# Kernel tuning notes

Measured on AMD Instinct MI355X. Metric: run time of the kernel, lower is better.

The kernel has to match this reference:

```python
import jax, jax.numpy as jnp
import numpy as np

BS, SL, INDIM, D, H = 2, 2048, 1024, 64, 16
DH = D * H


def _rotation_buffers(sl, units):
    # int rotation_values branch: values=arange(sl), min_lam=1, max_lam=1000
    half = units // 2
    min_lam, max_lam = 1.0, 1000.0
    theta = min_lam / (2.0 * np.pi) * (max_lam / min_lam) ** (2.0 * np.arange(half) / units)
    pos = np.arange(sl, dtype=np.float64)[:, None] / theta[None]  # [sl, half]
    # tile([...,2]).reshape == repeat each entry twice along last dim -> [sl, units]
    rcos = np.repeat(np.cos(pos), 2, axis=-1).astype(np.float32)
    rsin = np.repeat(np.sin(pos), 2, axis=-1).astype(np.float32)
    return jnp.asarray(rcos), jnp.asarray(rsin)


def setup_inputs() -> dict:
    key = jax.random.key(0)
    ks = jax.random.split(key, 8)
    s = 0.02
    x = jax.random.normal(ks[0], (BS, SL, INDIM), jnp.float32)
    mask = jnp.zeros((BS, SL), jnp.float32)  # subtracted from logits; zeros = no masking
    Wqkv = jax.random.normal(ks[1], (INDIM, 3 * DH), jnp.float32) * s
    bqkv = jnp.zeros((3 * DH,), jnp.float32)
    Wo = jax.random.normal(ks[2], (DH, INDIM), jnp.float32) * s
    bo = jnp.zeros((INDIM,), jnp.float32)
    Wg = jax.random.normal(ks[3], (INDIM, DH), jnp.float32) * s
    bg = jnp.zeros((DH,), jnp.float32)
    Wb = jax.random.normal(ks[4], (INDIM, H), jnp.float32) * s
    bb = jnp.zeros((H,), jnp.float32)
    alphaq = jnp.zeros((), jnp.float32)
    alphak = jnp.zeros((), jnp.float32)
    alphav = jnp.zeros((), jnp.float32)
    rcos, rsin = _rotation_buffers(SL, D)
    return dict(x=x, mask=mask, Wqkv=Wqkv, bqkv=bqkv, Wo=Wo, bo=bo, Wg=Wg, bg=bg,
                Wb=Wb, bb=bb, alphaq=alphaq, alphak=alphak, alphav=alphav,
                rcos=rcos, rsin=rsin)


def _rotate(X, cos, sin_even):
    # Faithful to the in-place torch code:
    #   X_ = X*cos; X_[...,::2] += -sin[...,::2]*X_[...,1::2];
    #   X_[...,1::2] += sin[...,::2]*X_[...,::2]   (uses UPDATED even lanes)
    Xc = X * cos
    even = Xc[..., 0::2] - sin_even * Xc[..., 1::2]
    odd = Xc[..., 1::2] + sin_even * even
    return jnp.stack([even, odd], axis=-1).reshape(X.shape)


def reference(x, mask, Wqkv, bqkv, Wo, bo, Wg, bg, Wb, bb, alphaq, alphak, alphav, rcos, rsin):
    bs, sl, _ = x.shape
    qkv = x @ Wqkv + bqkv  # [bs, sl, 3*DH]
    Q, K, V = jnp.split(qkv, 3, axis=-1)
    # split last dim as (d, h) and move heads out: [bs, h, sl, d]
    def split_heads(t):
        return t.reshape(bs, sl, D, H).transpose(0, 3, 1, 2)
    Q = split_heads(Q) * jax.nn.sigmoid(alphaq)
    K = split_heads(K) * jax.nn.sigmoid(alphak)
    V = split_heads(V) * jax.nn.sigmoid(alphav)
    cos = rcos[:sl]            # [sl, d]
    sin_even = rsin[:sl, 0::2]  # [sl, d/2]
    Q = _rotate(Q, cos, sin_even)
    K = _rotate(K, cos, sin_even)
    scale = D ** (-0.5)
    QK = scale * jnp.einsum('bhqd,bhkd->bhqk', Q, K)  # [bs,h,sl,sl]
    # 'regular' bias: Wb(x) -> [bs,sl,h] -> [bs,h,1,sl] broadcast over queries
    B = (x @ Wb + bb)
    QK = QK + jnp.transpose(B, (0, 2, 1))[:, :, None, :]
    QK = QK - mask[:, None, None, :]
    w = jax.nn.softmax(QK, axis=-1)
    att = jnp.einsum('bhqk,bhkd->bhqd', w, V)  # [bs,h,sl,d]
    # sigmoid gate, split the same (d,h) way
    G = jax.nn.sigmoid(x @ Wg + bg).reshape(bs, sl, D, H).transpose(0, 3, 1, 2)
    att = att * G
    # merge heads back as (d, h) -> [bs, sl, d*h]
    att = att.transpose(0, 2, 3, 1).reshape(bs, sl, DH)
    resid = att @ Wo + bo
    return x + resid  # identity shortcut (out_units == indim), dropout=0
```

## Files before the change

kernel.cpp:

```cpp
#include <hip/hip_runtime.h>
#include <cstdint>

typedef unsigned short u16;
typedef unsigned int   u32;
typedef __bf16 bf16x8 __attribute__((ext_vector_type(8)));
typedef u16    u16x8  __attribute__((ext_vector_type(8)));
typedef float  f32x4  __attribute__((ext_vector_type(4)));
typedef float  f32x16 __attribute__((ext_vector_type(16)));
typedef u32    u32x2v __attribute__((ext_vector_type(2)));
typedef __attribute__((address_space(3))) void lds_void;
typedef __attribute__((address_space(1))) void gl_void;

#define GLDS16(gsrc, ldst) \
  __builtin_amdgcn_global_load_lds((gl_void*)(gsrc), (lds_void*)(ldst), 16, 0, 0)

#define DEV __device__ __forceinline__
#define LOG2E 1.4426950408889634f

DEV u16 f2bf(float f) {
  uint32_t u = __float_as_uint(f);
  u += 0x7fff + ((u >> 16) & 1);
  return (u16)(u >> 16);
}
DEV float bf2f(u16 h) { return __uint_as_float(((uint32_t)h) << 16); }
DEV float sigm(float x) { return 1.0f / (1.0f + __expf(-x)); }

DEV void wtrans_body(const float* __restrict__ W, u16* __restrict__ Wt, int K, int N,
                     int kt, int nt, int t, float (*tile)[33], int perm) {
  int r = t >> 5, c = t & 31;
#pragma unroll
  for (int i = 0; i < 4; ++i)
    tile[r + i * 8][c] = W[(size_t)(kt * 32 + r + i * 8) * N + nt * 32 + c];
  __syncthreads();
#pragma unroll
  for (int i = 0; i < 4; ++i) {
    int ko = kt * 32 + c;
    int kdst = perm ? ((ko & 15) * 64 + (ko >> 4)) : ko;
    Wt[(size_t)(nt * 32 + r + i * 8) * K + kdst] = f2bf(tile[c][r + i * 8]);
  }
}

__global__ __launch_bounds__(256) void prep_k(const float* __restrict__ x,
    const float* __restrict__ Wqkv, const float* __restrict__ Wg, const float* __restrict__ Wo,
    const float* __restrict__ Wb, const float* __restrict__ bb, const float* __restrict__ mask,
    u16* __restrict__ xb, u16* __restrict__ wcat, u16* __restrict__ wo_t2,
    float* __restrict__ bmT) {
  __shared__ float tile[32][33];
  const int bid = blockIdx.x, t = threadIdx.x;
  if (bid < 4096) {
    int i = bid * 256 + t;
    float4 v = ((const float4*)x)[i];
    ushort4 o;
    o.x = f2bf(v.x); o.y = f2bf(v.y); o.z = f2bf(v.z); o.w = f2bf(v.w);
    ((ushort4*)xb)[i] = o;
  } else if (bid < 7168) {
    int b2 = bid - 4096;
    wtrans_body(Wqkv, wcat, 1024, 3072, b2 & 31, b2 >> 5, t, tile, 0);
  } else if (bid < 8192) {
    int b2 = bid - 7168;
    wtrans_body(Wg, wcat + (size_t)3072 * 1024, 1024, 1024, b2 & 31, b2 >> 5, t, tile, 0);
  } else if (bid < 9216) {
    int b2 = bid - 8192;
    wtrans_body(Wo, wo_t2, 1024, 1024, b2 & 31, b2 >> 5, t, tile, 1);
  } else {
    int row = (bid - 9216) * 4 + (t >> 6);
    int l = t & 63;
    const float* xr = x + (size_t)row * 1024;
    float acc[16];
#pragma unroll
    for (int h = 0; h < 16; ++h) acc[h] = 0.f;
    for (int it = 0; it < 16; ++it) {
      int k = l + it * 64;
      float xv = xr[k];
      const float4* wr = (const float4*)(Wb + k * 16);
#pragma unroll
      for (int q = 0; q < 4; ++q) {
        float4 wv = wr[q];
        acc[q * 4 + 0] += xv * wv.x; acc[q * 4 + 1] += xv * wv.y;
        acc[q * 4 + 2] += xv * wv.z; acc[q * 4 + 3] += xv * wv.w;
      }
    }
#pragma unroll
    for (int h = 0; h < 16; ++h) {
      float v = acc[h];
#pragma unroll
      for (int m = 32; m >= 1; m >>= 1) v += __shfl_xor(v, m, 64);
      acc[h] = v;
    }
    if (l < 16) {
      int b = row >> 11, s = row & 2047;
      bmT[(size_t)(b * 16 + l) * 2048 + s] = (acc[l] + bb[l] - mask[row]) * LOG2E;
    }
  }
}

__global__ __launch_bounds__(256) void gemmF_k(const u16* __restrict__ A, const u16* __restrict__ Bt,
                                               const float* __restrict__ bqkv, const float* __restrict__ bg,
                                               u16* __restrict__ qkvb, u16* __restrict__ gh_rm) {
  __shared__ u16 sAB[4][2][4096];
  const int t = threadIdx.x, w = t >> 6, l = t & 63;
  const int lr = l & 15, lg = l >> 4;
  const int bm = blockIdx.x, bn = blockIdx.y;
  const int wr = w >> 1, wc = w & 1;
  f32x4 acc[4][4] = {};

  auto stage = [&](int buf, int kt) {
    kt &= 31;
    u16* As = &sAB[buf][0][0];
    u16* Bs = &sAB[buf][1][0];
#pragma unroll
    for (int r = 0; r < 2; ++r) {
      int L = r * 256 + t;
      GLDS16(A + (size_t)(bm * 128 + (L >> 2)) * 1024 + (kt * 32 + (L & 3) * 8),
             &As[(r * 256 + w * 64) * 8]);
      GLDS16(Bt + (size_t)(bn * 128 + (L >> 2)) * 1024 + (kt * 32 + (L & 3) * 8),
             &Bs[(r * 256 + w * 64) * 8]);
    }
  };

  stage(0, 0);
  stage(1, 1);
#pragma unroll 4
  for (int kt = 0; kt < 32; ++kt) {
    const int buf = kt & 3;
    stage((kt + 2) & 3, kt + 2);
    asm volatile("s_waitcnt vmcnt(8)" ::: "memory");
    __builtin_amdgcn_s_barrier();
    __builtin_amdgcn_sched_barrier(0);
    const u16* As = &sAB[buf][0][0];
    const u16* Bs = &sAB[buf][1][0];
    bf16x8 af[4], bfr[4];
#pragma unroll
    for (int m = 0; m < 4; ++m) af[m] = *(const bf16x8*)&As[(wr * 64 + m * 16 + lr) * 32 + lg * 8];
#pragma unroll
    for (int n = 0; n < 4; ++n) bfr[n] = *(const bf16x8*)&Bs[(wc * 64 + n * 16 + lr) * 32 + lg * 8];
#pragma unroll
    for (int m = 0; m < 4; ++m)
#pragma unroll
      for (int n = 0; n < 4; ++n)
        acc[m][n] = __builtin_amdgcn_mfma_f32_16x16x32_bf16(af[m], bfr[n], acc[m][n], 0, 0, 0);
  }
  asm volatile("s_waitcnt vmcnt(0)" ::: "memory");
#pragma unroll
  for (int m = 0; m < 4; ++m)
#pragma unroll
    for (int n = 0; n < 4; ++n) {
      int col = bn * 128 + wc * 64 + n * 16 + lr;
      float bv = (bn < 24) ? bqkv[col] : bg[col - 3072];
#pragma unroll
      for (int rg = 0; rg < 4; ++rg) {
        int row = bm * 128 + wr * 64 + m * 16 + lg * 4 + rg;
        float v = acc[m][n][rg] + bv;
        if (bn < 24) qkvb[(size_t)row * 3072 + col] = f2bf(v);
        else         gh_rm[(size_t)row * 1024 + (col - 3072)] = f2bf(sigm(v));
      }
    }
}

__global__ __launch_bounds__(256) void relayout_k(const u16* __restrict__ qkv,
    const u16* __restrict__ gh_rm,
    const float* __restrict__ rcos, const float* __restrict__ rsin,
    const float* __restrict__ aq, const float* __restrict__ ak, const float* __restrict__ av,
    u16* __restrict__ Qh, u16* __restrict__ Kh, u16* __restrict__ Vh, u16* __restrict__ Gh) {
  int row = blockIdx.x;
  int b = row >> 11, s = row & 2047;
  int t = threadIdx.x;
  float sq = sigm(*aq) * 0.125f * LOG2E, sk = sigm(*ak), sv = sigm(*av);
  const u16* qrow = qkv + (size_t)row * 3072;
  if (t < 128) {
    int which = t >> 6;
    int idx = t & 63;
    int hoct = idx & 1, dp = idx >> 1;
    const u16* src = qrow + which * 1024;
    float sc = which ? sk : sq;
    u16* dst = which ? Kh : Qh;
    float cc = rcos[s * 64 + 2 * dp];
    float sn = rsin[s * 64 + 2 * dp];
    u16x8 Av = *(const u16x8*)(src + dp * 32 + hoct * 8);
    u16x8 Bv = *(const u16x8*)(src + dp * 32 + 16 + hoct * 8);
#pragma unroll
    for (int j = 0; j < 8; ++j) {
      float xe = bf2f(Av[j]) * sc, xo = bf2f(Bv[j]) * sc;
      float e = cc * xe - sn * (cc * xo);
      float o2 = cc * xo + sn * e;
      u32 pk = (u32)f2bf(e) | ((u32)f2bf(o2) << 16);
      *(u32*)&dst[((size_t)(b * 16 + hoct * 8 + j) * 2048 + s) * 64 + 2 * dp] = pk;
    }
  }
  {
    const u16* src = qrow + 2048;
    int h = t >> 4, d0 = (t & 15) * 4;
    ushort4 o4;
    o4.x = f2bf(bf2f(src[(d0 + 0) * 16 + h]) * sv);
    o4.y = f2bf(bf2f(src[(d0 + 1) * 16 + h]) * sv);
    o4.z = f2bf(bf2f(src[(d0 + 2) * 16 + h]) * sv);
    o4.w = f2bf(bf2f(src[(d0 + 3) * 16 + h]) * sv);
    *(ushort4*)&Vh[((size_t)(b * 16 + h) * 2048 + s) * 64 + d0] = o4;
  }
  {
    const u16* src = gh_rm + (size_t)row * 1024;
    int h = t >> 4, d0 = (t & 15) * 4;
    ushort4 o4;
    o4.x = src[(d0 + 0) * 16 + h];
    o4.y = src[(d0 + 1) * 16 + h];
    o4.z = src[(d0 + 2) * 16 + h];
    o4.w = src[(d0 + 3) * 16 + h];
    *(ushort4*)&Gh[((size_t)(b * 16 + h) * 2048 + s) * 64 + d0] = o4;
  }
}

__global__ __launch_bounds__(256) void vtrans_k(const u16* __restrict__ Vh, u16* __restrict__ VTg) {
  __shared__ u16 vt[4096];
  int bh = blockIdx.x, kt = blockIdx.y;
  int t = threadIdx.x;
  {
    int kp = t >> 3, dc = t & 7;
    const u16* vsrc = Vh + ((size_t)bh * 2048 + kt * 64 + kp * 2) * 64 + dc * 8;
    u16x8 v0 = *(const u16x8*)vsrc;
    u16x8 v1 = *(const u16x8*)(vsrc + 64);
#pragma unroll
    for (int j = 0; j < 8; ++j) {
      int d = dc * 8 + j;
      int sw = (d & 7) ^ ((d >> 3) & 7);
      *(u32*)((char*)vt + d * 128 + ((kp * 4) ^ (sw << 4))) = (u32)v0[j] | ((u32)v1[j] << 16);
    }
  }
  __syncthreads();
  {
    int d = t >> 2, ch = t & 3;
    int sw = (d & 7) ^ ((d >> 3) & 7);
    u16x8 a = *(const u16x8*)((const char*)vt + d * 128 + ((ch ^ sw) << 4));
    u16x8 b = *(const u16x8*)((const char*)vt + d * 128 + (((ch + 4) ^ sw) << 4));
    u16* dst = VTg + ((size_t)bh * 64 + d) * 2048 + kt * 64;
    *(u16x8*)(dst + ch * 8) = a;
    *(u16x8*)(dst + (ch + 4) * 8) = b;
  }
}

__global__ __launch_bounds__(256) void attn6_k(const u16* __restrict__ Qh, const u16* __restrict__ Kh,
    const u16* __restrict__ VTg, const float* __restrict__ bmT, const u16* __restrict__ Gh,
    u16* __restrict__ attg2) {
  __shared__ u16 smem[16384];
  const int t = threadIdx.x, w = t >> 6, l = t & 63;
  const int q32 = l & 31, hi = l >> 5;
  const int bid = blockIdx.x;
  const int xcd = bid & 7, within = bid >> 3;
  const int bh = xcd * 4 + (within & 3);
  const int qt = within >> 2;
  const int q0w = qt * 128 + w * 32;

  bf16x8 qf[4];
  {
    const u16* qbase = Qh + ((size_t)bh * 2048 + q0w + q32) * 64 + hi * 8;
#pragma unroll
    for (int ks = 0; ks < 4; ++ks) qf[ks] = *(const bf16x8*)(qbase + ks * 16);
  }
  union { u32 wd[4]; bf16x8 v; } onesf;
  onesf.wd[0] = 0x3F803F80u; onesf.wd[1] = 0x3F803F80u;
  onesf.wd[2] = 0x3F803F80u; onesf.wd[3] = 0x3F803F80u;

  f32x16 o0 = {}, o1 = {};
  f32x16 liacc = {};

  auto stage = [&](int buf, int kt) {
    u16* KsT = smem + buf * 8192;
    u16* VTsT = KsT + 4096;
#pragma unroll
    for (int r = 0; r < 2; ++r) {
      int L = r * 256 + t;
      int row = L >> 3, kc = L & 7;
      GLDS16(Kh + ((size_t)bh * 2048 + kt * 64 + row) * 64 + ((kc ^ (row & 7)) * 8),
             &KsT[(r * 256 + w * 64) * 8]);
    }
#pragma unroll
    for (int r = 0; r < 2; ++r) {
      int L = r * 256 + t;
      int d = L >> 3, kc = L & 7;
      GLDS16(VTg + ((size_t)bh * 64 + d) * 2048 + kt * 64 + ((kc ^ (d & 7)) * 8),
             &VTsT[(r * 256 + w * 64) * 8]);
    }
  };

  const float* bmb = bmT + (size_t)bh * 2048;
  stage(0, 0);
  float bv0 = bmb[q32], bv1 = bmb[32 + q32];
  __syncthreads();

  for (int kt = 0; kt < 32; ++kt) {
    const int buf = kt & 1;
    if (kt < 31) stage(buf ^ 1, kt + 1);
    float nb0 = 0.f, nb1 = 0.f;
    if (kt < 31) { nb0 = bmb[(kt + 1) * 64 + q32]; nb1 = bmb[(kt + 1) * 64 + 32 + q32]; }
    const u16* Ks = smem + buf * 8192;
    const u16* VTs = Ks + 4096;
#pragma unroll
    for (int sub = 0; sub < 2; ++sub) {
      union { u32 wd[4]; bf16x8 v; } Ab = {}, Bb = {};
      float bvs = sub ? bv1 : bv0;
      u32 bvb;
      asm("v_cvt_pk_bf16_f32 %0, %1, %2" : "=v"(bvb) : "v"(bvs), "v"(0.f));
      Ab.wd[0] = hi ? 0u : bvb;
      Bb.wd[0] = hi ? 0u : 0x3F80u;
      f32x16 s = {};
      s = __builtin_amdgcn_mfma_f32_32x32x16_bf16(Ab.v, Bb.v, s, 0, 0, 0);
#pragma unroll
      for (int ks = 0; ks < 4; ++ks) {
        bf16x8 kf = *(const bf16x8*)((const char*)Ks + (sub * 32 + q32) * 128 +
                                     (((2 * ks + hi) ^ (q32 & 7)) << 4));
        s = __builtin_amdgcn_mfma_f32_32x32x16_bf16(kf, qf[ks], s, 0, 0, 0);
      }
      float p[16];
#pragma unroll
      for (int r = 0; r < 16; ++r) p[r] = exp2f(s[r]);
      u32 c[8];
#pragma unroll
      for (int i2 = 0; i2 < 8; ++i2)
        asm("v_cvt_pk_bf16_f32 %0, %1, %2" : "=v"(c[i2]) : "v"(p[2 * i2]), "v"(p[2 * i2 + 1]));
      asm volatile("v_permlane32_swap_b32 %0, %1" : "+v"(c[0]), "+v"(c[2]));
      asm volatile("v_permlane32_swap_b32 %0, %1" : "+v"(c[1]), "+v"(c[3]));
      asm volatile("v_permlane32_swap_b32 %0, %1" : "+v"(c[4]), "+v"(c[6]));
      asm volatile("v_permlane32_swap_b32 %0, %1" : "+v"(c[5]), "+v"(c[7]));
      union { u32 wd[4]; bf16x8 v; } pf0, pf1;
      pf0.wd[0] = c[0]; pf0.wd[1] = c[1]; pf0.wd[2] = c[2]; pf0.wd[3] = c[3];
      pf1.wd[0] = c[4]; pf1.wd[1] = c[5]; pf1.wd[2] = c[6]; pf1.wd[3] = c[7];
      liacc = __builtin_amdgcn_mfma_f32_32x32x16_bf16(onesf.v, pf0.v, liacc, 0, 0, 0);
      liacc = __builtin_amdgcn_mfma_f32_32x32x16_bf16(onesf.v, pf1.v, liacc, 0, 0, 0);
#pragma unroll
      for (int ks2 = 0; ks2 < 2; ++ks2) {
        int chunk = sub * 4 + ks2 * 2 + hi;
        const bf16x8* pv = ks2 ? &pf1.v : &pf0.v;
        {
          int d = q32;
          bf16x8 vf = *(const bf16x8*)((const char*)VTs + d * 128 + ((chunk ^ (d & 7)) << 4));
          o0 = __builtin_amdgcn_mfma_f32_32x32x16_bf16(vf, *pv, o0, 0, 0, 0);
        }
        {
          int d = 32 + q32;
          bf16x8 vf = *(const bf16x8*)((const char*)VTs + d * 128 + ((chunk ^ (d & 7)) << 4));
          o1 = __builtin_amdgcn_mfma_f32_32x32x16_bf16(vf, *pv, o1, 0, 0, 0);
        }
      }
    }
    __syncthreads();
    bv0 = nb0; bv1 = nb1;
  }
  float inv = 1.f / liacc[0];
#pragma unroll
  for (int r = 0; r < 16; ++r) { o0[r] *= inv; o1[r] *= inv; }
  {
    char* ob = (char*)smem + w * 4096;
#pragma unroll
    for (int dt = 0; dt < 2; ++dt) {
#pragma unroll
      for (int rq = 0; rq < 4; ++rq) {
        int dbase = rq * 8 + hi * 4 + dt * 32;
        float e0v = dt ? o1[rq * 4 + 0] : o0[rq * 4 + 0];
        float e1v = dt ? o1[rq * 4 + 1] : o0[rq * 4 + 1];
        float e2v = dt ? o1[rq * 4 + 2] : o0[rq * 4 + 2];
        float e3v = dt ? o1[rq * 4 + 3] : o0[rq * 4 + 3];
        u32 lo = (u32)f2bf(e0v) | ((u32)f2bf(e1v) << 16);
        u32 h2 = (u32)f2bf(e2v) | ((u32)f2bf(e3v) << 16);
        u32x2v val = {lo, h2};
        *(u32x2v*)(ob + q32 * 128 + ((dbase * 2) ^ ((q32 & 7) << 4))) = val;
      }
    }
    const u16* gbase = Gh + ((size_t)bh * 2048 + q0w) * 64;
    u16* abase = attg2 + ((size_t)bh * 2048 + q0w) * 64;
#pragma unroll
    for (int cc = 0; cc < 4; ++cc) {
      int off16 = cc * 64 + l;
      int q = off16 >> 3;
      int inner = (off16 & 7) << 4;
      u16x8 ov = *(const u16x8*)(ob + q * 128 + (inner ^ ((q & 7) << 4)));
      u16x8 gv = *(const u16x8*)(gbase + off16 * 8);
      u16x8 outv;
#pragma unroll
      for (int jj = 0; jj < 8; ++jj) outv[jj] = f2bf(bf2f(ov[jj]) * bf2f(gv[jj]));
      *(u16x8*)(abase + off16 * 8) = outv;
    }
  }
}

__global__ __launch_bounds__(256) void gemm2_k(const u16* __restrict__ A, const u16* __restrict__ Bt,
                                               const float* __restrict__ bo, const float* __restrict__ x,
                                               float* __restrict__ out) {
  __shared__ u16 sA[4][2048];
  __shared__ u16 sB[4][4096];
  const int t = threadIdx.x, w = t >> 6, l = t & 63;
  const int lr = l & 15, lg = l >> 4;
  const int bm = blockIdx.x, bn = blockIdx.y;
  const int wr = w >> 1, wc = w & 1;
  f32x4 acc[2][4] = {};

  auto stage = [&](int buf, int kt) {
    kt &= 31;
    {
      int arow = bm * 64 + (t >> 2), ak = kt * 32 + (t & 3) * 8;
      size_t aoff = ((size_t)((arow >> 11) * 16 + (ak >> 6)) * 2048 + (arow & 2047)) * 64 + (ak & 63);
      GLDS16(A + aoff, &sA[buf][w * 64 * 8]);
    }
#pragma unroll
    for (int r = 0; r < 2; ++r) {
      int L = r * 256 + t;
      GLDS16(Bt + (size_t)(bn * 128 + (L >> 2)) * 1024 + (kt * 32 + (L & 3) * 8),
             &sB[buf][(r * 256 + w * 64) * 8]);
    }
  };

  stage(0, 0);
  stage(1, 1);
#pragma unroll 4
  for (int kt = 0; kt < 32; ++kt) {
    const int buf = kt & 3;
    stage((kt + 2) & 3, kt + 2);
    asm volatile("s_waitcnt vmcnt(6)" ::: "memory");
    __builtin_amdgcn_s_barrier();
    __builtin_amdgcn_sched_barrier(0);
    bf16x8 af[2], bfr[4];
#pragma unroll
    for (int m = 0; m < 2; ++m) af[m] = *(const bf16x8*)&sA[buf][(wr * 32 + m * 16 + lr) * 32 + lg * 8];
#pragma unroll
    for (int n = 0; n < 4; ++n) bfr[n] = *(const bf16x8*)&sB[buf][(wc * 64 + n * 16 + lr) * 32 + lg * 8];
#pragma unroll
    for (int m = 0; m < 2; ++m)
#pragma unroll
      for (int n = 0; n < 4; ++n)
        acc[m][n] = __builtin_amdgcn_mfma_f32_16x16x32_bf16(af[m], bfr[n], acc[m][n], 0, 0, 0);
  }
  asm volatile("s_waitcnt vmcnt(0)" ::: "memory");
#pragma unroll
  for (int m = 0; m < 2; ++m)
#pragma unroll
    for (int n = 0; n < 4; ++n) {
      int col = bn * 128 + wc * 64 + n * 16 + lr;
      float bv = bo[col];
#pragma unroll
      for (int rg = 0; rg < 4; ++rg) {
        int row = bm * 64 + wr * 32 + m * 16 + lg * 4 + rg;
        out[(size_t)row * 1024 + col] = acc[m][n][rg] + bv + x[(size_t)row * 1024 + col];
      }
    }
}

extern "C" void kernel_launch(void* const* d_in, const int* in_sizes, int n_in,
                              void* d_out, int out_size, void* d_ws, size_t ws_size,
                              hipStream_t stream) {
  (void)in_sizes; (void)n_in; (void)out_size; (void)ws_size;
  const float* x    = (const float*)d_in[0];
  const float* mask = (const float*)d_in[1];
  const float* Wqkv = (const float*)d_in[2];
  const float* bqkv = (const float*)d_in[3];
  const float* Wo   = (const float*)d_in[4];
  const float* bo   = (const float*)d_in[5];
  const float* Wg   = (const float*)d_in[6];
  const float* bg   = (const float*)d_in[7];
  const float* Wb   = (const float*)d_in[8];
  const float* bb   = (const float*)d_in[9];
  const float* aq   = (const float*)d_in[10];
  const float* ak   = (const float*)d_in[11];
  const float* av   = (const float*)d_in[12];
  const float* rcos = (const float*)d_in[13];
  const float* rsin = (const float*)d_in[14];
  float* out = (float*)d_out;

  char* ws = (char*)d_ws;
  size_t o = 0;
  u16* x_bf   = (u16*)(ws + o); o += (size_t)4096 * 1024 * 2;
  u16* wcat   = (u16*)(ws + o); o += (size_t)4096 * 1024 * 2;
  u16* wo_t2  = (u16*)(ws + o); o += (size_t)1024 * 1024 * 2;
  u16* qkv_b  = (u16*)(ws + o); o += (size_t)4096 * 3072 * 2;
  u16* gh_rm  = (u16*)(ws + o); o += (size_t)4096 * 1024 * 2;
  u16* Gh     = (u16*)(ws + o); o += (size_t)32 * 2048 * 64 * 2;
  u16* Qh     = (u16*)(ws + o); o += (size_t)32 * 2048 * 64 * 2;
  u16* Kh     = (u16*)(ws + o); o += (size_t)32 * 2048 * 64 * 2;
  u16* Vh     = (u16*)(ws + o); o += (size_t)32 * 2048 * 64 * 2;
  u16* VTg    = (u16*)(ws + o); o += (size_t)32 * 64 * 2048 * 2;
  float* bmT  = (float*)(ws + o); o += (size_t)32 * 2048 * 4;
  u16* attg2  = Vh;

  prep_k<<<10240, 256, 0, stream>>>(x, Wqkv, Wg, Wo, Wb, bb, mask, x_bf, wcat, wo_t2, bmT);
  gemmF_k<<<dim3(32, 32), 256, 0, stream>>>(x_bf, wcat, bqkv, bg, qkv_b, gh_rm);
  relayout_k<<<4096, 256, 0, stream>>>(qkv_b, gh_rm, rcos, rsin, aq, ak, av, Qh, Kh, Vh, Gh);
  vtrans_k<<<dim3(32, 32), 256, 0, stream>>>(Vh, VTg);
  attn6_k<<<512, 256, 0, stream>>>(Qh, Kh, VTg, bmT, Gh, attg2);
  gemm2_k<<<dim3(64, 8), 256, 0, stream>>>(attg2, wo_t2, bo, x, out);
}
```

Before: 279.8 us.

## Split attention KV range across two wave groups per block and merge in LDS

The attention kernel moves from 256 to 512 threads per block. Two groups of four waves each process half of the key/value sequence for the same 128 queries, each with its own double-buffered LDS staging. At the end, the second group writes its unnormalized outputs and row sums to LDS, and the first group adds them and normalizes before the gated store. The aim is more waves in flight per query tile and a shorter serial KV loop, at the cost of twice the LDS per block and an extra reduction pass with a barrier.

```diff
diff --git a/kernel.cpp b/kernel.cpp
--- a/kernel.cpp
+++ b/kernel.cpp
@@ -237,17 +237,20 @@
   }
 }
 
-__global__ __launch_bounds__(256) void attn6_k(const u16* __restrict__ Qh, const u16* __restrict__ Kh,
+__global__ __launch_bounds__(512) void attn7_k(const u16* __restrict__ Qh, const u16* __restrict__ Kh,
     const u16* __restrict__ VTg, const float* __restrict__ bmT, const u16* __restrict__ Gh,
     u16* __restrict__ attg2) {
-  __shared__ u16 smem[16384];
+  __shared__ u16 smem[32768];
   const int t = threadIdx.x, w = t >> 6, l = t & 63;
   const int q32 = l & 31, hi = l >> 5;
+  const int kvh = w >> 2, wq = w & 3;
+  const int tl = t & 255, wl = tl >> 6;
   const int bid = blockIdx.x;
   const int xcd = bid & 7, within = bid >> 3;
   const int bh = xcd * 4 + (within & 3);
   const int qt = within >> 2;
-  const int q0w = qt * 128 + w * 32;
+  const int q0w = qt * 128 + wq * 32;
+  const int kb0 = kvh * 1024;
 
   bf16x8 qf[4];
   {
@@ -262,36 +265,37 @@
   f32x16 o0 = {}, o1 = {};
   f32x16 liacc = {};
 
-  auto stage = [&](int buf, int kt) {
-    u16* KsT = smem + buf * 8192;
+  auto stage = [&](int buf, int step) {
+    u16* KsT = smem + (kvh * 2 + buf) * 8192;
     u16* VTsT = KsT + 4096;
+    int kb = kb0 + step * 64;
 #pragma unroll
     for (int r = 0; r < 2; ++r) {
-      int L = r * 256 + t;
+      int L = r * 256 + tl;
       int row = L >> 3, kc = L & 7;
-      GLDS16(Kh + ((size_t)bh * 2048 + kt * 64 + row) * 64 + ((kc ^ (row & 7)) * 8),
-             &KsT[(r * 256 + w * 64) * 8]);
+      GLDS16(Kh + ((size_t)bh * 2048 + kb + row) * 64 + ((kc ^ (row & 7)) * 8),
+             &KsT[(r * 256 + wl * 64) * 8]);
     }
 #pragma unroll
     for (int r = 0; r < 2; ++r) {
-      int L = r * 256 + t;
+      int L = r * 256 + tl;
       int d = L >> 3, kc = L & 7;
-      GLDS16(VTg + ((size_t)bh * 64 + d) * 2048 + kt * 64 + ((kc ^ (d & 7)) * 8),
-             &VTsT[(r * 256 + w * 64) * 8]);
+      GLDS16(VTg + ((size_t)bh * 64 + d) * 2048 + kb + ((kc ^ (d & 7)) * 8),
+             &VTsT[(r * 256 + wl * 64) * 8]);
     }
   };
 
-  const float* bmb = bmT + (size_t)bh * 2048;
+  const float* bmb = bmT + (size_t)bh * 2048 + kb0;
   stage(0, 0);
   float bv0 = bmb[q32], bv1 = bmb[32 + q32];
   __syncthreads();
 
-  for (int kt = 0; kt < 32; ++kt) {
-    const int buf = kt & 1;
-    if (kt < 31) stage(buf ^ 1, kt + 1);
+  for (int step = 0; step < 16; ++step) {
+    const int buf = step & 1;
+    if (step < 15) stage(buf ^ 1, step + 1);
     float nb0 = 0.f, nb1 = 0.f;
-    if (kt < 31) { nb0 = bmb[(kt + 1) * 64 + q32]; nb1 = bmb[(kt + 1) * 64 + 32 + q32]; }
-    const u16* Ks = smem + buf * 8192;
+    if (step < 15) { nb0 = bmb[(step + 1) * 64 + q32]; nb1 = bmb[(step + 1) * 64 + 32 + q32]; }
+    const u16* Ks = smem + (kvh * 2 + buf) * 8192;
     const u16* VTs = Ks + 4096;
 #pragma unroll
     for (int sub = 0; sub < 2; ++sub) {
@@ -344,11 +348,29 @@
     __syncthreads();
     bv0 = nb0; bv1 = nb1;
   }
-  float inv = 1.f / liacc[0];
-#pragma unroll
-  for (int r = 0; r < 16; ++r) { o0[r] *= inv; o1[r] *= inv; }
-  {
-    char* ob = (char*)smem + w * 4096;
+
+  if (kvh == 1) {
+    float* Of = (float*)smem + wq * 2048;
+#pragma unroll
+    for (int r = 0; r < 16; ++r) {
+      int d = (r & 3) + 8 * (r >> 2) + 4 * hi;
+      Of[d * 32 + q32] = o0[r];
+      Of[(d + 32) * 32 + q32] = o1[r];
+    }
+    if (hi == 0) ((float*)((char*)smem + 32768))[wq * 32 + q32] = liacc[0];
+  }
+  __syncthreads();
+  if (kvh == 0) {
+    const float* Of = (const float*)smem + wq * 2048;
+    float liB = ((const float*)((char*)smem + 32768))[wq * 32 + q32];
+    float inv = 1.f / (liacc[0] + liB);
+#pragma unroll
+    for (int r = 0; r < 16; ++r) {
+      int d = (r & 3) + 8 * (r >> 2) + 4 * hi;
+      o0[r] = (o0[r] + Of[d * 32 + q32]) * inv;
+      o1[r] = (o1[r] + Of[(d + 32) * 32 + q32]) * inv;
+    }
+    char* ob = (char*)smem + 36864 + wq * 4096;
 #pragma unroll
     for (int dt = 0; dt < 2; ++dt) {
 #pragma unroll
@@ -482,6 +504,6 @@
   gemmF_k<<<dim3(32, 32), 256, 0, stream>>>(x_bf, wcat, bqkv, bg, qkv_b, gh_rm);
   relayout_k<<<4096, 256, 0, stream>>>(qkv_b, gh_rm, rcos, rsin, aq, ak, av, Qh, Kh, Vh, Gh);
   vtrans_k<<<dim3(32, 32), 256, 0, stream>>>(Vh, VTg);
-  attn6_k<<<512, 256, 0, stream>>>(Qh, Kh, VTg, bmT, Gh, attg2);
+  attn7_k<<<512, 512, 0, stream>>>(Qh, Kh, VTg, bmT, Gh, attg2);
   gemm2_k<<<dim3(64, 8), 256, 0, stream>>>(attg2, wo_t2, bo, x, out);
 }
```

Result: no change. 282.7 us (+1.1%).
